# Kernel optimization log

Measured on AMD Instinct MI355X. Metric: run time of the kernel, lower is better.

## Reference

```python
import jax, jax.numpy as jnp
from jax import lax
import numpy as np

B = 2048; IMG = 28; K = 3; CIN = 1; HC = 32; LC = 16; WID = 64; HID = 64
LIS = IMG - 3 * (K - 1)           # 22: latent image size
FLAT = LIS * LIS * HC             # 15488
BLK = WID * LC                    # 1024: hypernet block size
T1 = 10.0; T0 = 0.0; NSTEP = 20   # fixed-step RK4 replaces adaptive dopri5
VAR = 0.1                         # p_z0 diagonal covariance


def _conv(x, w, b):  # w: [Cout,Cin,k,k], VALID conv, stride 1
    y = lax.conv_general_dilated(x, w, (1, 1), 'VALID',
                                 dimension_numbers=('NCHW', 'OIHW', 'NCHW'))
    return y + b[None, :, None, None]


def _convT(x, w, b):  # w: [Cin,Cout,k,k] (pytorch ConvTranspose2d layout)
    wf = jnp.flip(w, (2, 3)).transpose(1, 0, 2, 3)  # -> OIHW, spatially flipped
    y = lax.conv_general_dilated(x, wf, (1, 1), [(K - 1, K - 1), (K - 1, K - 1)],
                                 dimension_numbers=('NCHW', 'OIHW', 'NCHW'))
    return y + b[None, :, None, None]


def _forward(x, c0w, c0b, c1w, c1b, c2w, c2b, elw, elb, dlw, dlb,
             t0w, t0b, t1w, t1b, t2w, t2b, h1w, h1b, h2w, h2b, h3w, h3b):
    # ---- encoder (dropout in eval = identity) ----
    h = jnp.tanh(_conv(x, c0w, c0b))
    h = jnp.tanh(_conv(h, c1w, c1b))
    h = jnp.tanh(_conv(h, c2w, c2b))
    z1 = h.reshape(h.shape[0], -1) @ elw + elb          # [B, LC]
    # ---- decoder ----
    d = jnp.tanh(z1 @ dlw + dlb)                         # [B, FLAT]
    d = d.reshape(-1, HC, LIS, LIS)
    d = jnp.tanh(_convT(d, t0w, t0b))
    d = jnp.tanh(_convT(d, t1w, t1b))
    recon = _convT(d, t2w, t2b)                          # [B, CIN, 28, 28]

    # ---- CNF vector field with analytic trace ----
    def hyper(t):
        p = jnp.tanh(jnp.reshape(jnp.asarray(t, jnp.float32), (1, 1)) @ h1w + h1b)
        p = jnp.tanh(p @ h2w + h2b)
        p = (p @ h3w + h3b).reshape(-1)
        W = p[:BLK].reshape(WID, LC)
        U = p[BLK:2 * BLK].reshape(WID, LC) * jax.nn.sigmoid(p[2 * BLK:3 * BLK].reshape(WID, LC))
        Bb = p[3 * BLK:]                                 # [WID]
        return W, Bb, U

    def f(t, z):
        W, Bb, U = hyper(t)
        hh = jnp.tanh(jnp.einsum('bd,wd->wb', z, W) + Bb[:, None])   # [WID, B]
        dz = jnp.einsum('wb,wd->bd', hh, U) / WID                     # [B, LC]
        s = jnp.sum(W * U, axis=1)                                    # [WID]: sum_i W_w[i]U_w[i]
        tr = jnp.mean((1.0 - hh * hh) * s[:, None], axis=0)           # [B] analytic trace
        return dz, -tr[:, None]

    dt = (T0 - T1) / NSTEP

    def step(state, i):
        z, lp = state
        t = T1 + i * dt
        k1z, k1l = f(t, z)
        k2z, k2l = f(t + 0.5 * dt, z + 0.5 * dt * k1z)
        k3z, k3l = f(t + 0.5 * dt, z + 0.5 * dt * k2z)
        k4z, k4l = f(t + dt, z + dt * k3z)
        z = z + dt / 6.0 * (k1z + 2 * k2z + 2 * k3z + k4z)
        lp = lp + dt / 6.0 * (k1l + 2 * k2l + 2 * k3l + k4l)
        return (z, lp), None

    lp1 = jnp.zeros((z1.shape[0], 1), z1.dtype)
    (z0, lp0), _ = lax.scan(step, (z1, lp1), jnp.arange(NSTEP, dtype=jnp.float32))

    # MultivariateNormal(0, 0.1*I) log_prob
    logp = -0.5 * (LC * jnp.log(2 * jnp.pi) + LC * jnp.log(VAR) + jnp.sum(z0 * z0, -1) / VAR)
    x_probs = jnp.mean(logp - lp0[:, 0])
    return recon, x_probs


def setup_inputs() -> dict:
    key = jax.random.key(0)
    ks = jax.random.split(key, 16)
    n = jax.random.normal
    s = jnp.float32(0.05)
    z = jnp.zeros
    OUT3 = 3 * BLK + WID
    return {
        'x': n(ks[0], (B, CIN, IMG, IMG), jnp.float32),
        'c0w': n(ks[1], (HC, CIN, K, K)) * s, 'c0b': z((HC,)),
        'c1w': n(ks[2], (HC, HC, K, K)) * s, 'c1b': z((HC,)),
        'c2w': n(ks[3], (HC, HC, K, K)) * s, 'c2b': z((HC,)),
        'elw': n(ks[4], (FLAT, LC)) * s, 'elb': z((LC,)),
        'dlw': n(ks[5], (LC, FLAT)) * s, 'dlb': z((FLAT,)),
        't0w': n(ks[6], (HC, HC, K, K)) * s, 't0b': z((HC,)),
        't1w': n(ks[7], (HC, HC, K, K)) * s, 't1b': z((HC,)),
        't2w': n(ks[8], (HC, CIN, K, K)) * s, 't2b': z((CIN,)),
        'h1w': n(ks[9], (1, HID)) * s, 'h1b': z((HID,)),
        'h2w': n(ks[10], (HID, HID)) * s, 'h2b': z((HID,)),
        'h3w': n(ks[11], (HID, OUT3)) * s, 'h3b': z((OUT3,)),
    }


def reference(x, c0w, c0b, c1w, c1b, c2w, c2b, elw, elb, dlw, dlb,
              t0w, t0b, t1w, t1b, t2w, t2b, h1w, h1b, h2w, h2b, h3w, h3b):
    return _forward(x, c0w, c0b, c1w, c1b, c2w, c2b, elw, elb, dlw, dlb,
                    t0w, t0b, t1w, t1b, t2w, t2b, h1w, h1b, h2w, h2b, h3w, h3b)
```

## Files before the change

### kernel.cpp

```cpp
#include <hip/hip_runtime.h>
#include <math.h>

#define Bsz 2048

using bf16x8 = __attribute__((ext_vector_type(8))) short;
using f32x4  = __attribute__((ext_vector_type(4))) float;

__device__ __forceinline__ float fast_tanh(float x){
    float e = __expf(2.0f * x);
    return 1.0f - 2.0f / (e + 1.0f);
}
__device__ __forceinline__ float fast_sigmoid(float x){
    return 1.0f / (1.0f + __expf(-x));
}
__device__ __forceinline__ unsigned short f2b(float f){
    union { float f; unsigned u; } v; v.f = f;
    unsigned r = v.u + 0x7FFFu + ((v.u >> 16) & 1u);
    return (unsigned short)(r >> 16);
}
__device__ __forceinline__ float b2f(unsigned short s){
    union { unsigned u; float f; } v; v.u = ((unsigned)s) << 16;
    return v.f;
}

__device__ __forceinline__ float stage_t(int sidx){
    int i  = sidx >> 2, st = sidx & 3;
    float t = 10.0f - 0.5f * (float)i;
    if (st == 1 || st == 2) t -= 0.25f;
    else if (st == 3)       t -= 0.5f;
    return t;
}

__global__ void k_prep(const float* __restrict__ c1w, const float* __restrict__ c2w,
                       const float* __restrict__ t0w, const float* __restrict__ t1w,
                       const float* __restrict__ elw, const float* __restrict__ dlw,
                       const float* __restrict__ elb, const float* __restrict__ dlb,
                       const float* __restrict__ t2w,
                       unsigned short* __restrict__ wc1, unsigned short* __restrict__ wc2,
                       unsigned short* __restrict__ wt0, unsigned short* __restrict__ wt1,
                       unsigned short* __restrict__ t2wPk,
                       unsigned short* __restrict__ elwT, unsigned short* __restrict__ dlwT,
                       float* __restrict__ dlbT, float* __restrict__ z1, int full){
    int gsz = gridDim.x * 256;
    for (int i = blockIdx.x*256 + threadIdx.x; i < 9216; i += gsz){
        int ci = i & 31, co = (i >> 5) & 31, s = i >> 10;
        wc1[i] = f2b(c1w[(co*32 + ci)*9 + s]);
        wc2[i] = f2b(c2w[(co*32 + ci)*9 + s]);
        wt0[i] = f2b(t0w[(ci*32 + co)*9 + (8 - s)]);
        wt1[i] = f2b(t1w[(ci*32 + co)*9 + (8 - s)]);
    }
    if (!full) return;
    for (int i = blockIdx.x*256 + threadIdx.x; i < 288; i += gsz){
        int tap = i >> 5, ci = i & 31;
        int r = tap / 3, s = tap - r*3;
        t2wPk[i] = f2b(t2w[ci*9 + (2-r)*3 + (2-s)]);
    }
    for (int i = blockIdx.x*256 + threadIdx.x; i < 32768; i += gsz)
        z1[i] = elb[i & 15];
    for (int i = blockIdx.x*256 + threadIdx.x; i < 15488; i += gsz){
        int pos = i >> 5, ci = i & 31;
        dlbT[i] = dlb[ci*484 + pos];
    }
    for (int i = blockIdx.x*256 + threadIdx.x; i < 247808; i += gsz){
        int l = i / 15488, f2 = i - l*15488;
        int pos = f2 >> 5, ci = f2 & 31;
        elwT[i] = f2b(elw[(ci*484 + pos)*16 + l]);
    }
    for (int i = blockIdx.x*256 + threadIdx.x; i < 247808; i += gsz){
        int f2 = i >> 4, l = i & 15;
        int pos = f2 >> 5, ci = f2 & 31;
        dlwT[i] = f2b(dlw[l*15488 + ci*484 + pos]);
    }
}

__global__ void __launch_bounds__(256)
k_enc01(const float* __restrict__ x, const float* __restrict__ c0w,
        const float* __restrict__ c0b, const unsigned short* __restrict__ wc1,
        const float* __restrict__ c1b, unsigned short* __restrict__ A1,
        int cb){
    __shared__ __align__(16) unsigned short A0L[676*36];
    const int tid = threadIdx.x, b = blockIdx.x;
    const float* xin = x + (size_t)(cb + b)*784;

    for (int pos = tid; pos < 676; pos += 256){
        int y = pos / 26, xx = pos - y*26;
        float v[9];
#pragma unroll
        for (int r = 0; r < 3; r++)
#pragma unroll
            for (int s = 0; s < 3; s++)
                v[r*3+s] = xin[(y+r)*28 + xx + s];
        float acc[32];
#pragma unroll
        for (int co = 0; co < 32; co++) acc[co] = c0b[co];
#pragma unroll
        for (int k = 0; k < 9; k++)
#pragma unroll
            for (int co = 0; co < 32; co++)
                acc[co] += v[k] * c0w[co*9 + k];
        unsigned short* ob = A0L + pos*36;
#pragma unroll
        for (int g = 0; g < 8; g++){
            ushort4 o;
            o.x = f2b(fast_tanh(acc[g*4+0])); o.y = f2b(fast_tanh(acc[g*4+1]));
            o.z = f2b(fast_tanh(acc[g*4+2])); o.w = f2b(fast_tanh(acc[g*4+3]));
            *(ushort4*)(ob + g*4) = o;
        }
    }
    __syncthreads();

    const int wave = tid >> 6, lane = tid & 63;
    const int q = lane >> 4, nn = lane & 15;
    bf16x8 af[2][9];
#pragma unroll
    for (int mt = 0; mt < 2; mt++)
#pragma unroll
        for (int s = 0; s < 9; s++)
            af[mt][s] = *(const bf16x8*)(wc1 + s*1024 + (mt*16 + nn)*32 + q*8);
    float4 bc0 = *(const float4*)(c1b + q*4);
    float4 bc1 = *(const float4*)(c1b + 16 + q*4);
    unsigned short* outb = A1 + (size_t)b*25088;

    for (int t = wave; t < 36; t += 4){
        int pos = t*16 + nn;
        int oy = pos / 24, ox = pos - oy*24;
        const unsigned short* ib = A0L + (oy*26 + ox)*36 + q*8;
        f32x4 acc0 = {0.f,0.f,0.f,0.f}, acc1 = {0.f,0.f,0.f,0.f};
#pragma unroll
        for (int r = 0; r < 3; r++){
            bf16x8 b0 = *(const bf16x8*)(ib + (r*26 + 0)*36);
            bf16x8 b1 = *(const bf16x8*)(ib + (r*26 + 1)*36);
            bf16x8 b2 = *(const bf16x8*)(ib + (r*26 + 2)*36);
            acc0 = __builtin_amdgcn_mfma_f32_16x16x32_bf16(af[0][r*3+0], b0, acc0, 0,0,0);
            acc1 = __builtin_amdgcn_mfma_f32_16x16x32_bf16(af[1][r*3+0], b0, acc1, 0,0,0);
            acc0 = __builtin_amdgcn_mfma_f32_16x16x32_bf16(af[0][r*3+1], b1, acc0, 0,0,0);
            acc1 = __builtin_amdgcn_mfma_f32_16x16x32_bf16(af[1][r*3+1], b1, acc1, 0,0,0);
            acc0 = __builtin_amdgcn_mfma_f32_16x16x32_bf16(af[0][r*3+2], b2, acc0, 0,0,0);
            acc1 = __builtin_amdgcn_mfma_f32_16x16x32_bf16(af[1][r*3+2], b2, acc1, 0,0,0);
        }
        int opix = oy*24 + ox;
        ushort4 o0, o1;
        o0.x = f2b(fast_tanh(acc0[0] + bc0.x)); o0.y = f2b(fast_tanh(acc0[1] + bc0.y));
        o0.z = f2b(fast_tanh(acc0[2] + bc0.z)); o0.w = f2b(fast_tanh(acc0[3] + bc0.w));
        o1.x = f2b(fast_tanh(acc1[0] + bc1.x)); o1.y = f2b(fast_tanh(acc1[1] + bc1.y));
        o1.z = f2b(fast_tanh(acc1[2] + bc1.z)); o1.w = f2b(fast_tanh(acc1[3] + bc1.w));
        *(ushort4*)(outb + opix*32 + q*4)      = o0;
        *(ushort4*)(outb + opix*32 + 16 + q*4) = o1;
    }
}

template<int IL, int OL, int OW, int OOFF, int INS, int OUTS>
__global__ void __launch_bounds__(256)
k_convM(const unsigned short* __restrict__ in, const unsigned short* __restrict__ wg,
        const float* __restrict__ bias, unsigned short* __restrict__ out, int CH){
    constexpr int N  = OL * OL;
    constexpr int NT = (N + 15) / 16;
    const int tid = threadIdx.x;
    const int wave = tid >> 6, lane = tid & 63;
    const int q = lane >> 4, nn = lane & 15;
    const int nw = gridDim.x * 4;

    bf16x8 af[2][9];
#pragma unroll
    for (int mt = 0; mt < 2; mt++)
#pragma unroll
        for (int s = 0; s < 9; s++)
            af[mt][s] = *(const bf16x8*)(wg + s*1024 + (mt*16 + nn)*32 + q*8);
    float4 bc0 = *(const float4*)(bias + q*4);
    float4 bc1 = *(const float4*)(bias + 16 + q*4);

    for (int t = blockIdx.x*4 + wave; t < CH*NT; t += nw){
        int img = t / NT, tt = t - img*NT;
        const unsigned short* inb = in + (size_t)img * INS;
        unsigned short* outb = out + (size_t)img * OUTS;
        int pos = tt*16 + nn;
        int pc  = pos < N ? pos : N - 1;
        int oy = pc / OL, ox = pc - oy*OL;
        const unsigned short* ib = inb + (oy*IL + ox)*32 + q*8;
        f32x4 acc0 = {0.f,0.f,0.f,0.f}, acc1 = {0.f,0.f,0.f,0.f};
#pragma unroll
        for (int r = 0; r < 3; r++){
            bf16x8 b0 = *(const bf16x8*)(ib + (r*IL + 0)*32);
            bf16x8 b1 = *(const bf16x8*)(ib + (r*IL + 1)*32);
            bf16x8 b2 = *(const bf16x8*)(ib + (r*IL + 2)*32);
            acc0 = __builtin_amdgcn_mfma_f32_16x16x32_bf16(af[0][r*3+0], b0, acc0, 0,0,0);
            acc1 = __builtin_amdgcn_mfma_f32_16x16x32_bf16(af[1][r*3+0], b0, acc1, 0,0,0);
            acc0 = __builtin_amdgcn_mfma_f32_16x16x32_bf16(af[0][r*3+1], b1, acc0, 0,0,0);
            acc1 = __builtin_amdgcn_mfma_f32_16x16x32_bf16(af[1][r*3+1], b1, acc1, 0,0,0);
            acc0 = __builtin_amdgcn_mfma_f32_16x16x32_bf16(af[0][r*3+2], b2, acc0, 0,0,0);
            acc1 = __builtin_amdgcn_mfma_f32_16x16x32_bf16(af[1][r*3+2], b2, acc1, 0,0,0);
        }
        if (pos < N){
            int opix = oy*OW + ox + OOFF;
            ushort4 o0, o1;
            o0.x = f2b(fast_tanh(acc0[0] + bc0.x)); o0.y = f2b(fast_tanh(acc0[1] + bc0.y));
            o0.z = f2b(fast_tanh(acc0[2] + bc0.z)); o0.w = f2b(fast_tanh(acc0[3] + bc0.w));
            o1.x = f2b(fast_tanh(acc1[0] + bc1.x)); o1.y = f2b(fast_tanh(acc1[1] + bc1.y));
            o1.z = f2b(fast_tanh(acc1[2] + bc1.z)); o1.w = f2b(fast_tanh(acc1[3] + bc1.w));
            *(ushort4*)(outb + opix*32 + q*4)      = o0;
            *(ushort4*)(outb + opix*32 + 16 + q*4) = o1;
        }
    }
}

__global__ void __launch_bounds__(256)
k_encg(const unsigned short* __restrict__ A2, const unsigned short* __restrict__ elwT,
       float* __restrict__ z1, int cb, int CH){
    int wave = threadIdx.x >> 6, lane = threadIdx.x & 63;
    int q = lane >> 4, nn = lane & 15;
    int imgb = blockIdx.x*16;
    const unsigned short* ap = A2 + (size_t)(imgb + nn)*15488 + q*8;
    const unsigned short* bp = elwT + (size_t)nn*15488 + q*8;
    f32x4 acc = {0.f,0.f,0.f,0.f};
    int s0 = blockIdx.y*121;
#pragma unroll 2
    for (int s = s0 + wave; s < s0 + 121; s += 4){
        bf16x8 a = *(const bf16x8*)(ap + s*32);
        bf16x8 b = *(const bf16x8*)(bp + s*32);
        acc = __builtin_amdgcn_mfma_f32_16x16x32_bf16(a, b, acc, 0,0,0);
    }
    float* zp = z1 + (size_t)(cb + imgb)*16;
#pragma unroll
    for (int i = 0; i < 4; i++)
        atomicAdd(zp + (q*4 + i)*16 + nn, acc[i]);
}

__global__ void __launch_bounds__(256)
k_decgM(const float* __restrict__ z1, const unsigned short* __restrict__ dlwT,
        const float* __restrict__ dlbT, unsigned short* __restrict__ D0c, int cb){
    __shared__ float zb[16*17];
    const int tid = threadIdx.x;
    const int wave = tid >> 6, lane = tid & 63;
    const int q = lane >> 4, n = lane & 15;
    const int imgb = blockIdx.y*16;
    zb[(tid >> 4)*17 + (tid & 15)] = z1[(size_t)(cb + imgb + (tid >> 4))*16 + (tid & 15)];
    __syncthreads();

    bf16x8 zf;
    if (q < 2){
        unsigned short tmp[8];
#pragma unroll
        for (int j = 0; j < 8; j++) tmp[j] = f2b(zb[n*17 + q*8 + j]);
        zf = *(bf16x8*)tmp;
    } else {
        bf16x8 zz = {0,0,0,0,0,0,0,0}; zf = zz;
    }

#pragma unroll
    for (int ii = 0; ii < 4; ii++){
        int mt = blockIdx.x*16 + wave*4 + ii;
        if (mt >= 968) break;
        int mb = mt*16;
        bf16x8 afr;
        if (q < 2) afr = *(const bf16x8*)(dlwT + (size_t)(mb + n)*16 + q*8);
        else { bf16x8 zz = {0,0,0,0,0,0,0,0}; afr = zz; }
        f32x4 acc = {0.f,0.f,0.f,0.f};
        acc = __builtin_amdgcn_mfma_f32_16x16x32_bf16(afr, zf, acc, 0,0,0);
        float4 bias = *(const float4*)(dlbT + mb + q*4);
        ushort4 o;
        o.x = f2b(fast_tanh(acc[0] + bias.x));
        o.y = f2b(fast_tanh(acc[1] + bias.y));
        o.z = f2b(fast_tanh(acc[2] + bias.z));
        o.w = f2b(fast_tanh(acc[3] + bias.w));
        *(ushort4*)(D0c + (size_t)(imgb + n)*15488 + mb + q*4) = o;
    }
}

struct PM {
    bf16x8 Wf[4];
    bf16x8 Uf[2];
    float4 Bbf[4];
    float4 sf[4];
    float stot;
};
__device__ __forceinline__ void loadPM(const float* __restrict__ g, int lane, int q, PM& p){
    const unsigned short* gW = (const unsigned short*)g;
    const unsigned short* gU = (const unsigned short*)(g + 1024);
#pragma unroll
    for (int c = 0; c < 4; c++)
        p.Wf[c] = *(const bf16x8*)(gW + (c*64 + lane)*8);
#pragma unroll
    for (int kb = 0; kb < 2; kb++)
        p.Uf[kb] = *(const bf16x8*)(gU + (kb*64 + lane)*8);
#pragma unroll
    for (int c = 0; c < 4; c++){
        p.Bbf[c] = *(const float4*)(g + 1536 + c*16 + q*4);
        p.sf[c]  = *(const float4*)(g + 1600 + c*16 + q*4);
    }
    p.stot = g[1664];
}

__device__ __forceinline__ void cnf_body(const float* __restrict__ z1,
                                         const float* __restrict__ hyp,
                                         float* __restrict__ part, int bid,
                                         unsigned short* zsb, unsigned short* hhT){
    const int lane = threadIdx.x;
    const int q = lane >> 4, d = lane & 15;
    const float dt = -0.5f;

    float z[4], zacc[4], lacc[4], lp[4];
#pragma unroll
    for (int i = 0; i < 4; i++){
        z[i] = z1[(size_t)(bid*16 + q*4 + i)*16 + d];
        zacc[i] = 0.f; lacc[i] = 0.f; lp[i] = 0.f;
        zsb[(q*4 + i)*24 + d] = f2b(z[i]);
    }
    PM pm0, pm1;
    loadPM(hyp, lane, q, pm0);

#pragma unroll 2
    for (int sidx = 0; sidx < 80; sidx++){
        PM& cur = (sidx & 1) ? pm1 : pm0;
        PM& nxt = (sidx & 1) ? pm0 : pm1;
        if (sidx < 79) loadPM(hyp + (size_t)(sidx + 1)*2048, lane, q, nxt);

        bf16x8 zb;
        if (q < 2) zb = *(const bf16x8*)(zsb + d*24 + q*8);
        else { bf16x8 zz2 = {0,0,0,0,0,0,0,0}; zb = zz2; }

        f32x4 h0 = {0,0,0,0}, h1 = {0,0,0,0}, h2 = {0,0,0,0}, h3 = {0,0,0,0};
        h0 = __builtin_amdgcn_mfma_f32_16x16x32_bf16(cur.Wf[0], zb, h0, 0,0,0);
        h1 = __builtin_amdgcn_mfma_f32_16x16x32_bf16(cur.Wf[1], zb, h1, 0,0,0);
        h2 = __builtin_amdgcn_mfma_f32_16x16x32_bf16(cur.Wf[2], zb, h2, 0,0,0);
        h3 = __builtin_amdgcn_mfma_f32_16x16x32_bf16(cur.Wf[3], zb, h3, 0,0,0);

        float partial = 0.f;
        f32x4 hc[4] = {h0, h1, h2, h3};
#pragma unroll
        for (int c = 0; c < 4; c++){
            ushort4 o;
            float t0 = fast_tanh(hc[c][0] + cur.Bbf[c].x);
            float t1 = fast_tanh(hc[c][1] + cur.Bbf[c].y);
            float t2 = fast_tanh(hc[c][2] + cur.Bbf[c].z);
            float t3 = fast_tanh(hc[c][3] + cur.Bbf[c].w);
            partial += t0*t0*cur.sf[c].x + t1*t1*cur.sf[c].y
                     + t2*t2*cur.sf[c].z + t3*t3*cur.sf[c].w;
            o.x = f2b(t0); o.y = f2b(t1); o.z = f2b(t2); o.w = f2b(t3);
            *(ushort4*)(hhT + d*72 + c*16 + q*4) = o;
        }
        partial += __shfl_xor(partial, 16);
        partial += __shfl_xor(partial, 32);
        float trFull = (cur.stot - partial) * (1.f/64.f);

        bf16x8 a20 = *(const bf16x8*)(hhT + d*72 + q*8);
        bf16x8 a21 = *(const bf16x8*)(hhT + d*72 + 32 + q*8);
        f32x4 dzac = {0,0,0,0};
        dzac = __builtin_amdgcn_mfma_f32_16x16x32_bf16(a20, cur.Uf[0], dzac, 0,0,0);
        dzac = __builtin_amdgcn_mfma_f32_16x16x32_bf16(a21, cur.Uf[1], dzac, 0,0,0);

        int st = sidx & 3;
        float wgt = (st == 0 || st == 3) ? 1.f : 2.f;
#pragma unroll
        for (int i = 0; i < 4; i++){
            float dz = dzac[i] * (1.f/64.f);
            float dl = -__shfl(trFull, q*4 + i);
            zacc[i] += wgt * dz;
            lacc[i] += wgt * dl;
            float zsv;
            if (st < 3){
                float aa = (st == 2) ? 1.0f : 0.5f;
                zsv = z[i] + aa * dt * dz;
            } else {
                z[i]  += (dt/6.f) * zacc[i];
                lp[i] += (dt/6.f) * lacc[i];
                zsv = z[i];
                zacc[i] = 0.f; lacc[i] = 0.f;
            }
            zsb[(q*4 + i)*24 + d] = f2b(zsv);
        }
    }
    float sq[4];
#pragma unroll
    for (int i = 0; i < 4; i++) sq[i] = z[i]*z[i];
#pragma unroll
    for (int off = 1; off < 16; off <<= 1){
#pragma unroll
        for (int i = 0; i < 4; i++) sq[i] += __shfl_xor(sq[i], off, 16);
    }
    if (d == 0){
#pragma unroll
        for (int i = 0; i < 4; i++){
            float logp = -0.5f * (16.f*1.8378770664093453f
                                 + 16.f*(-2.302585092994046f) + sq[i]*10.f);
            part[bid*16 + q*4 + i] = logp - lp[i];
        }
    }
}

__global__ void __launch_bounds__(256)
k_dect0c(const unsigned short* __restrict__ D0c, const unsigned short* __restrict__ wt0,
         const float* __restrict__ t0b, unsigned short* __restrict__ D1,
         const float* __restrict__ z1, const float* __restrict__ hyp,
         float* __restrict__ part, int nCnf){
    __shared__ __align__(16) unsigned short D0L[676*36];
    __shared__ __align__(16) unsigned short zsbS[16*24];
    __shared__ __align__(16) unsigned short hhTS[16*72];
    const int tid = threadIdx.x;

    if (blockIdx.x < nCnf){
        if (tid >= 64) return;
        cnf_body(z1, hyp, part, blockIdx.x, zsbS, hhTS);
        return;
    }
    const int b = blockIdx.x - nCnf;
    unsigned short* d1b = D1 + (size_t)b*25088;
    {
        uint4 zq = {0,0,0,0};
        for (int p = tid; p < 676; p += 256){
            int y = p / 26, xx = p - y*26;
            if (y < 2 || y >= 24 || xx < 2 || xx >= 24){
                uint4* pt = (uint4*)(D0L + p*36);
                pt[0] = zq; pt[1] = zq; pt[2] = zq; pt[3] = zq;
            }
        }
        for (int p = tid; p < 784; p += 256){
            int y = p / 28, xx = p - y*28;
            if (y < 2 || y >= 26 || xx < 2 || xx >= 26){
                uint4* pt = (uint4*)(d1b + p*32);
                pt[0] = zq; pt[1] = zq; pt[2] = zq; pt[3] = zq;
            }
        }
    }
    {
        const uint4* src = (const uint4*)(D0c + (size_t)b*15488);
        for (int c = tid; c < 1936; c += 256){
            uint4 v = src[c];
            int pos = c >> 2, p8 = (c & 3)*8;
            int y = pos / 22, xx = pos - y*22;
            *(uint4*)(D0L + ((y+2)*26 + xx + 2)*36 + p8) = v;
        }
    }
    __syncthreads();

    const int wave = tid >> 6, lane = tid & 63;
    const int q = lane >> 4, nn = lane & 15;
    bf16x8 af[2][9];
#pragma unroll
    for (int mt = 0; mt < 2; mt++)
#pragma unroll
        for (int s = 0; s < 9; s++)
            af[mt][s] = *(const bf16x8*)(wt0 + s*1024 + (mt*16 + nn)*32 + q*8);
    float4 bc0 = *(const float4*)(t0b + q*4);
    float4 bc1 = *(const float4*)(t0b + 16 + q*4);

    for (int t = wave; t < 36; t += 4){
        int pos = t*16 + nn;
        int oy = pos / 24, ox = pos - oy*24;
        const unsigned short* ib = D0L + (oy*26 + ox)*36 + q*8;
        f32x4 acc0 = {0.f,0.f,0.f,0.f}, acc1 = {0.f,0.f,0.f,0.f};
#pragma unroll
        for (int r = 0; r < 3; r++){
            bf16x8 b0 = *(const bf16x8*)(ib + (r*26 + 0)*36);
            bf16x8 b1 = *(const bf16x8*)(ib + (r*26 + 1)*36);
            bf16x8 b2 = *(const bf16x8*)(ib + (r*26 + 2)*36);
            acc0 = __builtin_amdgcn_mfma_f32_16x16x32_bf16(af[0][r*3+0], b0, acc0, 0,0,0);
            acc1 = __builtin_amdgcn_mfma_f32_16x16x32_bf16(af[1][r*3+0], b0, acc1, 0,0,0);
            acc0 = __builtin_amdgcn_mfma_f32_16x16x32_bf16(af[0][r*3+1], b1, acc0, 0,0,0);
            acc1 = __builtin_amdgcn_mfma_f32_16x16x32_bf16(af[1][r*3+1], b1, acc1, 0,0,0);
            acc0 = __builtin_amdgcn_mfma_f32_16x16x32_bf16(af[0][r*3+2], b2, acc0, 0,0,0);
            acc1 = __builtin_amdgcn_mfma_f32_16x16x32_bf16(af[1][r*3+2], b2, acc1, 0,0,0);
        }
        int opix = oy*28 + ox + 58;
        ushort4 o0, o1;
        o0.x = f2b(fast_tanh(acc0[0] + bc0.x)); o0.y = f2b(fast_tanh(acc0[1] + bc0.y));
        o0.z = f2b(fast_tanh(acc0[2] + bc0.z)); o0.w = f2b(fast_tanh(acc0[3] + bc0.w));
        o1.x = f2b(fast_tanh(acc1[0] + bc1.x)); o1.y = f2b(fast_tanh(acc1[1] + bc1.y));
        o1.z = f2b(fast_tanh(acc1[2] + bc1.z)); o1.w = f2b(fast_tanh(acc1[3] + bc1.w));
        *(ushort4*)(d1b + opix*32 + q*4)      = o0;
        *(ushort4*)(d1b + opix*32 + 16 + q*4) = o1;
    }
}

__global__ void __launch_bounds__(256)
k_dect12(const unsigned short* __restrict__ D1, const unsigned short* __restrict__ wt1,
         const float* __restrict__ t1b, const unsigned short* __restrict__ t2wPk,
         const float* __restrict__ t2b, float* __restrict__ out,
         const float* __restrict__ part, int cb, int CH){
    __shared__ __align__(16) unsigned short D2L[900*40];
    const int tid = threadIdx.x, b = blockIdx.x;
    if (b >= CH){
        __shared__ float red[256];
        float s = 0.f;
#pragma unroll
        for (int k = 0; k < 8; k++) s += part[tid + k*256];
        red[tid] = s;
        __syncthreads();
        for (int st = 128; st > 0; st >>= 1){
            if (tid < st) red[tid] += red[tid + st];
            __syncthreads();
        }
        if (tid == 0) out[1605632] = red[0] * (1.f/2048.f);
        return;
    }
    const unsigned short* d1b = D1 + (size_t)b*25088;
    const int wave = tid >> 6, lane = tid & 63;
    const int q = lane >> 4, nn = lane & 15;

    {
        uint4 zq = {0,0,0,0};
        for (int p = tid; p < 900; p += 256){
            int y = p / 30, xx = p - y*30;
            if (y < 2 || y >= 28 || xx < 2 || xx >= 28){
                uint4* pt = (uint4*)(D2L + p*40);
                pt[0] = zq; pt[1] = zq; pt[2] = zq; pt[3] = zq;
            }
        }
    }
    {
        bf16x8 af[2][9];
#pragma unroll
        for (int mt = 0; mt < 2; mt++)
#pragma unroll
            for (int s = 0; s < 9; s++)
                af[mt][s] = *(const bf16x8*)(wt1 + s*1024 + (mt*16 + nn)*32 + q*8);
        float4 bc0 = *(const float4*)(t1b + q*4);
        float4 bc1 = *(const float4*)(t1b + 16 + q*4);

        for (int t = wave; t < 43; t += 4){
            int pos = t*16 + nn;
            int pc  = pos < 676 ? pos : 675;
            int oy = pc / 26, ox = pc - oy*26;
            const unsigned short* ib = d1b + (oy*28 + ox)*32 + q*8;
            f32x4 acc0 = {0.f,0.f,0.f,0.f}, acc1 = {0.f,0.f,0.f,0.f};
#pragma unroll
            for (int r = 0; r < 3; r++){
                bf16x8 b0 = *(const bf16x8*)(ib + (r*28 + 0)*32);
                bf16x8 b1 = *(const bf16x8*)(ib + (r*28 + 1)*32);
                bf16x8 b2 = *(const bf16x8*)(ib + (r*28 + 2)*32);
                acc0 = __builtin_amdgcn_mfma_f32_16x16x32_bf16(af[0][r*3+0], b0, acc0, 0,0,0);
                acc1 = __builtin_amdgcn_mfma_f32_16x16x32_bf16(af[1][r*3+0], b0, acc1, 0,0,0);
                acc0 = __builtin_amdgcn_mfma_f32_16x16x32_bf16(af[0][r*3+1], b1, acc0, 0,0,0);
                acc1 = __builtin_amdgcn_mfma_f32_16x16x32_bf16(af[1][r*3+1], b1, acc1, 0,0,0);
                acc0 = __builtin_amdgcn_mfma_f32_16x16x32_bf16(af[0][r*3+2], b2, acc0, 0,0,0);
                acc1 = __builtin_amdgcn_mfma_f32_16x16x32_bf16(af[1][r*3+2], b2, acc1, 0,0,0);
            }
            if (pos < 676){
                int opix = (oy + 2)*30 + ox + 2;
                ushort4 o0, o1;
                o0.x = f2b(fast_tanh(acc0[0] + bc0.x)); o0.y = f2b(fast_tanh(acc0[1] + bc0.y));
                o0.z = f2b(fast_tanh(acc0[2] + bc0.z)); o0.w = f2b(fast_tanh(acc0[3] + bc0.w));
                o1.x = f2b(fast_tanh(acc1[0] + bc1.x)); o1.y = f2b(fast_tanh(acc1[1] + bc1.y));
                o1.z = f2b(fast_tanh(acc1[2] + bc1.z)); o1.w = f2b(fast_tanh(acc1[3] + bc1.w));
                *(ushort4*)(D2L + opix*40 + q*4)      = o0;
                *(ushort4*)(D2L + opix*40 + 16 + q*4) = o1;
            }
        }
    }
    __syncthreads();

    {
        bf16x8 wf[9];
#pragma unroll
        for (int tap = 0; tap < 9; tap++)
            wf[tap] = *(const bf16x8*)(t2wPk + tap*32 + q*8);
        float t2b0 = t2b[0];
        for (int t = wave; t < 49; t += 4){
            int p = t*16 + nn;
            int y = p / 28, xx = p - y*28;
            const unsigned short* bbase = D2L + (y*30 + xx)*40 + q*8;
            f32x4 acc = {0.f,0.f,0.f,0.f};
#pragma unroll
            for (int r = 0; r < 3; r++){
                acc = __builtin_amdgcn_mfma_f32_16x16x32_bf16(wf[r*3+0],
                        *(const bf16x8*)(bbase + (r*30 + 0)*40), acc, 0,0,0);
                acc = __builtin_amdgcn_mfma_f32_16x16x32_bf16(wf[r*3+1],
                        *(const bf16x8*)(bbase + (r*30 + 1)*40), acc, 0,0,0);
                acc = __builtin_amdgcn_mfma_f32_16x16x32_bf16(wf[r*3+2],
                        *(const bf16x8*)(bbase + (r*30 + 2)*40), acc, 0,0,0);
            }
            if (q == 0)
                out[(size_t)(cb + b)*784 + p] = acc[0] + t2b0;
        }
    }
}

template<int LOUT, int INW, int OUTW, int OUTOFF>
__device__ __forceinline__ void conv_gemm(const unsigned short* __restrict__ Wg,
                                          const float* __restrict__ bias,
                                          const unsigned short* inL,
                                          unsigned short* outL, int tid){
    constexpr int N  = LOUT * LOUT;
    constexpr int NT = (N + 15) / 16;
    const int lane  = tid & 63;
    const int wave  = tid >> 6;
    const int mtile = wave & 1;
    const int quad  = lane >> 4;
    const int nn    = lane & 15;
    bf16x8 afr[9];
    const unsigned short* wp = Wg + (mtile*16 + nn)*32 + quad*8;
#pragma unroll
    for (int s = 0; s < 9; s++)
        afr[s] = *(const bf16x8*)(wp + s*1024);
    float4 bco = *(const float4*)(bias + mtile*16 + quad*4);
    for (int t = (wave >> 1); t < NT; t += 2){
        int pos = t*16 + nn;
        int pc  = pos < N ? pos : N - 1;
        int y = pc / LOUT, x = pc - y*LOUT;
        const unsigned short* ib = inL + (y*INW + x)*32 + quad*8;
        f32x4 acc = {0.f, 0.f, 0.f, 0.f};
#pragma unroll
        for (int r = 0; r < 3; r++)
#pragma unroll
            for (int s = 0; s < 3; s++)
                acc = __builtin_amdgcn_mfma_f32_16x16x32_bf16(
                        afr[r*3+s], *(const bf16x8*)(ib + (r*INW + s)*32), acc, 0, 0, 0);
        if (pos < N){
            ushort4 o;
            o.x = f2b(fast_tanh(acc[0] + bco.x));
            o.y = f2b(fast_tanh(acc[1] + bco.y));
            o.z = f2b(fast_tanh(acc[2] + bco.z));
            o.w = f2b(fast_tanh(acc[3] + bco.w));
            int opix = y*OUTW + x + OUTOFF;
            *(ushort4*)(outL + opix*32 + mtile*16 + quad*4) = o;
        }
    }
}

__global__ void __launch_bounds__(256)
k_enc_f(const float* __restrict__ x,
        const float* __restrict__ c0w, const float* __restrict__ c0b,
        const unsigned short* __restrict__ wc1, const float* __restrict__ c1b,
        const unsigned short* __restrict__ wc2, const float* __restrict__ c2b,
        const float* __restrict__ elw, const float* __restrict__ elb,
        float* __restrict__ z1){
    __shared__ float X[784];
    __shared__ __align__(16) unsigned short H0[21632];
    __shared__ __align__(16) unsigned short H1[18432];
    __shared__ __align__(16) unsigned short H2[15488];
    __shared__ float red[16*17];
    const int tid = threadIdx.x, b = blockIdx.x;
    for (int i = tid; i < 784; i += 256) X[i] = x[b*784 + i];
    __syncthreads();
    for (int pos = tid; pos < 676; pos += 256){
        int y = pos / 26, xx = pos - y*26;
        float v[9];
#pragma unroll
        for (int r = 0; r < 3; r++)
#pragma unroll
            for (int s = 0; s < 3; s++)
                v[r*3+s] = X[(y+r)*28 + xx + s];
#pragma unroll
        for (int g = 0; g < 8; g++){
            float a0 = c0b[g*4+0], a1 = c0b[g*4+1], a2 = c0b[g*4+2], a3 = c0b[g*4+3];
#pragma unroll
            for (int k = 0; k < 9; k++){
                a0 += v[k] * c0w[(g*4+0)*9 + k];
                a1 += v[k] * c0w[(g*4+1)*9 + k];
                a2 += v[k] * c0w[(g*4+2)*9 + k];
                a3 += v[k] * c0w[(g*4+3)*9 + k];
            }
            ushort4 o;
            o.x = f2b(fast_tanh(a0)); o.y = f2b(fast_tanh(a1));
            o.z = f2b(fast_tanh(a2)); o.w = f2b(fast_tanh(a3));
            *(ushort4*)(H0 + pos*32 + g*4) = o;
        }
    }
    __syncthreads();
    conv_gemm<24, 26, 24, 0>(wc1, c1b, H0, H1, tid);
    __syncthreads();
    conv_gemm<22, 24, 22, 0>(wc2, c2b, H1, H2, tid);
    __syncthreads();
    {
        int fg = tid >> 4, l = tid & 15;
        float a = 0.f;
        for (int ci = 0; ci < 32; ci++)
            for (int pos = fg; pos < 484; pos += 16)
                a += b2f(H2[pos*32 + ci]) * elw[(ci*484 + pos)*16 + l];
        red[fg*17 + l] = a;
        __syncthreads();
        if (tid < 16){
            float s = elb[tid];
#pragma unroll
            for (int g = 0; g < 16; g++) s += red[g*17 + tid];
            z1[b*16 + tid] = s;
        }
    }
}

__global__ void __launch_bounds__(256)
k_dec_f(const float* __restrict__ z1,
        const float* __restrict__ dlw, const float* __restrict__ dlb,
        const unsigned short* __restrict__ wt0, const float* __restrict__ t0b,
        const unsigned short* __restrict__ wt1, const float* __restrict__ t1b,
        const float* __restrict__ t2w, const float* __restrict__ t2b,
        float* __restrict__ out){
    __shared__ __align__(16) unsigned short D0[21632];
    __shared__ __align__(16) unsigned short D1[25088];
    __shared__ __align__(16) unsigned short D2[28800];
    const int tid = threadIdx.x, b = blockIdx.x;
    {
        uint4 zq = {0,0,0,0};
        for (int i = tid; i < 2704; i += 256) ((uint4*)D0)[i] = zq;
        for (int i = tid; i < 3136; i += 256) ((uint4*)D1)[i] = zq;
        for (int i = tid; i < 3600; i += 256) ((uint4*)D2)[i] = zq;
    }
    float zz[16];
#pragma unroll
    for (int l = 0; l < 16; l++) zz[l] = z1[b*16 + l];
    __syncthreads();
    for (int f = tid; f < 15488; f += 256){
        float a = dlb[f];
#pragma unroll
        for (int l = 0; l < 16; l++) a += zz[l] * dlw[l*15488 + f];
        int ci = f / 484, pos = f - ci*484;
        int y = pos / 22, xx = pos - y*22;
        D0[((y+2)*26 + xx + 2)*32 + ci] = f2b(fast_tanh(a));
    }
    __syncthreads();
    conv_gemm<24, 26, 28, 58>(wt0, t0b, D0, D1, tid);
    __syncthreads();
    conv_gemm<26, 28, 30, 62>(wt1, t1b, D1, D2, tid);
    __syncthreads();
    for (int o = tid; o < 784; o += 256){
        int y = o / 28, xx = o - y*28;
        float a = t2b[0];
#pragma unroll
        for (int r = 0; r < 3; r++)
#pragma unroll
            for (int s = 0; s < 3; s++){
                const unsigned short* pp = D2 + ((y+r)*30 + xx + s)*32;
                int wi = (2-r)*3 + (2-s);
#pragma unroll
                for (int g = 0; g < 4; g++){
                    bf16x8 h = *(const bf16x8*)(pp + g*8);
#pragma unroll
                    for (int j = 0; j < 8; j++)
                        a += b2f((unsigned short)h[j]) * t2w[(g*8+j)*9 + wi];
                }
            }
        out[(size_t)b*784 + o] = a;
    }
}

__global__ void __launch_bounds__(64)
k_hyp1(const float* __restrict__ h1w, const float* __restrict__ h1b,
       const float* __restrict__ h2w, const float* __restrict__ h2b,
       float* __restrict__ p2ws){
    __shared__ float p1l[64];
    int sidx = blockIdx.x, tid = threadIdx.x;
    float t = stage_t(sidx);
    p1l[tid] = fast_tanh(t * h1w[tid] + h1b[tid]);
    __syncthreads();
    float a0 = h2b[tid], a1 = 0.f, a2 = 0.f, a3 = 0.f;
#pragma unroll
    for (int k = 0; k < 64; k += 4){
        a0 += p1l[k]   * h2w[(k)*64   + tid];
        a1 += p1l[k+1] * h2w[(k+1)*64 + tid];
        a2 += p1l[k+2] * h2w[(k+2)*64 + tid];
        a3 += p1l[k+3] * h2w[(k+3)*64 + tid];
    }
    p2ws[sidx*64 + tid] = fast_tanh((a0 + a1) + (a2 + a3));
}

__global__ void __launch_bounds__(256)
k_hyp2(const float* __restrict__ p2ws, const float* __restrict__ h3w,
       const float* __restrict__ h3b, float* __restrict__ p3ws){
    __shared__ float p2l[64];
    int sidx = blockIdx.y, tid = threadIdx.x;
    if (tid < 64) p2l[tid] = p2ws[sidx*64 + tid];
    __syncthreads();
    int m = blockIdx.x*256 + tid;
    if (m >= 3136) return;
    const float* hp = h3w + m;
    float a0 = h3b[m], a1 = 0.f, a2 = 0.f, a3 = 0.f;
#pragma unroll
    for (int k = 0; k < 64; k += 4){
        a0 += p2l[k]   * hp[(size_t)(k)*3136];
        a1 += p2l[k+1] * hp[(size_t)(k+1)*3136];
        a2 += p2l[k+2] * hp[(size_t)(k+2)*3136];
        a3 += p2l[k+3] * hp[(size_t)(k+3)*3136];
    }
    p3ws[(size_t)sidx*3200 + m] = (a0 + a1) + (a2 + a3);
}

__global__ void __launch_bounds__(256)
k_hyp3(const float* __restrict__ p3ws, float* __restrict__ hyp){
    __shared__ float sred[64];
    int sidx = blockIdx.x, tid = threadIdx.x;
    const float* p3 = p3ws + (size_t)sidx*3200;
    float* g = hyp + (size_t)sidx*2048;
    unsigned short* gW = (unsigned short*)g;
    unsigned short* gU = (unsigned short*)(g + 1024);
    {
        int lane = tid & 63, c = tid >> 6;
        int q = lane >> 4, m = lane & 15;
        ushort4 o0 = {0,0,0,0}, o1 = {0,0,0,0};
        if (q < 2){
            const float* wp = p3 + (c*16 + m)*16 + q*8;
            o0.x = f2b(wp[0]); o0.y = f2b(wp[1]); o0.z = f2b(wp[2]); o0.w = f2b(wp[3]);
            o1.x = f2b(wp[4]); o1.y = f2b(wp[5]); o1.z = f2b(wp[6]); o1.w = f2b(wp[7]);
        }
        *(ushort4*)(gW + tid*8)     = o0;
        *(ushort4*)(gW + tid*8 + 4) = o1;
    }
    if (tid < 128){
        int lane = tid & 63, kb = tid >> 6;
        int q = lane >> 4, d = lane & 15;
        unsigned short uo[8];
#pragma unroll
        for (int j = 0; j < 8; j++){
            int w = kb*32 + q*8 + j;
            float u = p3[1024 + w*16 + d] * fast_sigmoid(p3[2048 + w*16 + d]);
            uo[j] = f2b(u);
        }
        *(ushort4*)(gU + tid*8)     = *(ushort4*)&uo[0];
        *(ushort4*)(gU + tid*8 + 4) = *(ushort4*)&uo[4];
    } else if (tid < 192){
        int w = tid - 128;
        g[1536 + w] = p3[3072 + w];
    } else {
        int w = tid - 192;
        float s = 0.f;
#pragma unroll
        for (int d = 0; d < 16; d++){
            float u = p3[1024 + w*16 + d] * fast_sigmoid(p3[2048 + w*16 + d]);
            s += p3[w*16 + d] * u;
        }
        g[1600 + w] = s;
        sred[w] = s;
    }
    __syncthreads();
    if (tid == 0){
        float st = 0.f;
#pragma unroll
        for (int w = 0; w < 64; w++) st += sred[w];
        g[1664] = st;
    }
}

__global__ void k_hyper(const float* __restrict__ h1w, const float* __restrict__ h1b,
                        const float* __restrict__ h2w, const float* __restrict__ h2b,
                        const float* __restrict__ h3w, const float* __restrict__ h3b,
                        float* __restrict__ hyp){
    int sidx = blockIdx.x;
    float t = stage_t(sidx);
    __shared__ float p1[64], p2[64];
    __shared__ float p3[3136];
    int tid = threadIdx.x;
    if (tid < 64) p1[tid] = fast_tanh(t * h1w[tid] + h1b[tid]);
    __syncthreads();
    if (tid < 64){
        float a = h2b[tid];
#pragma unroll
        for (int k = 0; k < 64; k++) a += p1[k] * h2w[k*64 + tid];
        p2[tid] = fast_tanh(a);
    }
    __syncthreads();
    for (int m = tid; m < 3136; m += 256){
        float a = h3b[m];
#pragma unroll
        for (int k = 0; k < 64; k++) a += p2[k] * h3w[k*3136 + m];
        p3[m] = a;
    }
    __syncthreads();
    float* g = hyp + (size_t)sidx * 2304;
    for (int m = tid; m < 1024; m += 256){
        g[m] = p3[m];
        float u = p3[1024 + m] * fast_sigmoid(p3[2048 + m]);
        g[1024 + (m & 15)*64 + (m >> 4)] = u;
        p3[1024 + m] = u;
    }
    if (tid < 64) g[2048 + tid] = p3[3072 + tid];
    __syncthreads();
    if (tid < 64){
        float s = 0.f;
#pragma unroll
        for (int d = 0; d < 16; d++) s += p3[tid*16 + d] * p3[1024 + tid*16 + d];
        g[2112 + tid] = s;
    }
}

struct PF { float4 Wr[4]; float4 Ur[4]; float Bb, sw; };
__device__ __forceinline__ void load_pf(const float* __restrict__ g,
                                        int lane, int q, int d, PF& p){
    const float4* w4 = (const float4*)(g + lane*16);
    p.Wr[0] = w4[0]; p.Wr[1] = w4[1]; p.Wr[2] = w4[2]; p.Wr[3] = w4[3];
    const float4* u4 = (const float4*)(g + 1024 + d*64 + q*16);
    p.Ur[0] = u4[0]; p.Ur[1] = u4[1]; p.Ur[2] = u4[2]; p.Ur[3] = u4[3];
    p.Bb = g[2048 + lane];
    p.sw = g[2112 + lane];
}
__global__ void __launch_bounds__(64)
k_cnf_f(const float* __restrict__ z1, const float* __restrict__ hyp,
        float* __restrict__ part){
    __shared__ __align__(16) float zsl[16];
    __shared__ __align__(16) float hhl[64];
    const int lane = threadIdx.x;
    const int q = lane >> 4, d = lane & 15;
    const float dt = -0.5f;
    float z  = z1[(size_t)blockIdx.x*16 + d];
    float zs = z;
    float lp = 0.f, zacc = 0.f, lacc = 0.f;
    if (lane < 16) zsl[lane] = zs;
    PF cur, nxt;
    load_pf(hyp, lane, q, d, cur);
    for (int sidx = 0; sidx < 80; sidx++){
        __syncthreads();
        if (sidx < 79) load_pf(hyp + (size_t)(sidx + 1)*2304, lane, q, d, nxt);
        const float4* zp = (const float4*)zsl;
        float4 z0 = zp[0], z1v = zp[1], z2 = zp[2], z3 = zp[3];
        float a = cur.Bb;
        a += z0.x*cur.Wr[0].x + z0.y*cur.Wr[0].y + z0.z*cur.Wr[0].z + z0.w*cur.Wr[0].w;
        a += z1v.x*cur.Wr[1].x + z1v.y*cur.Wr[1].y + z1v.z*cur.Wr[1].z + z1v.w*cur.Wr[1].w;
        a += z2.x*cur.Wr[2].x + z2.y*cur.Wr[2].y + z2.z*cur.Wr[2].z + z2.w*cur.Wr[2].w;
        a += z3.x*cur.Wr[3].x + z3.y*cur.Wr[3].y + z3.z*cur.Wr[3].z + z3.w*cur.Wr[3].w;
        float hh = fast_tanh(a);
        float e = (1.f - hh*hh) * cur.sw;
#pragma unroll
        for (int off = 1; off < 64; off <<= 1)
            e += __shfl_xor(e, off);
        hhl[lane] = hh;
        __syncthreads();
        const float4* hp = (const float4*)(hhl + q*16);
        float4 h0 = hp[0], h1 = hp[1], h2 = hp[2], h3 = hp[3];
        float dzp = 0.f;
        dzp += h0.x*cur.Ur[0].x + h0.y*cur.Ur[0].y + h0.z*cur.Ur[0].z + h0.w*cur.Ur[0].w;
        dzp += h1.x*cur.Ur[1].x + h1.y*cur.Ur[1].y + h1.z*cur.Ur[1].z + h1.w*cur.Ur[1].w;
        dzp += h2.x*cur.Ur[2].x + h2.y*cur.Ur[2].y + h2.z*cur.Ur[2].z + h2.w*cur.Ur[2].w;
        dzp += h3.x*cur.Ur[3].x + h3.y*cur.Ur[3].y + h3.z*cur.Ur[3].z + h3.w*cur.Ur[3].w;
        dzp += __shfl_xor(dzp, 16);
        dzp += __shfl_xor(dzp, 32);
        float dz = dzp * (1.f/64.f);
        float dl = -e  * (1.f/64.f);
        int st = sidx & 3;
        float wgt = (st == 0 || st == 3) ? 1.f : 2.f;
        zacc += wgt * dz;
        lacc += wgt * dl;
        if (st < 3){
            float aa = (st == 2) ? 1.0f : 0.5f;
            zs = z + aa * dt * dz;
        } else {
            z  += (dt/6.f) * zacc;
            lp += (dt/6.f) * lacc;
            zs = z;
            zacc = 0.f; lacc = 0.f;
        }
        if (lane < 16) zsl[lane] = zs;
        cur = nxt;
    }
    float sq = z * z;
#pragma unroll
    for (int off = 1; off < 16; off <<= 1) sq += __shfl_xor(sq, off, 16);
    float logp = -0.5f * (16.f*1.8378770664093453f + 16.f*(-2.302585092994046f) + sq*10.f);
    if (lane == 0) part[blockIdx.x] = logp - lp;
}

__global__ void k_final(const float* __restrict__ part, float* __restrict__ out){
    __shared__ float red[256];
    int tid = threadIdx.x;
    float s = 0.f;
#pragma unroll
    for (int k = 0; k < 8; k++) s += part[tid + k*256];
    red[tid] = s;
    __syncthreads();
    for (int st = 128; st > 0; st >>= 1){
        if (tid < st) red[tid] += red[tid + st];
        __syncthreads();
    }
    if (tid == 0) out[1605632] = red[0] * (1.f/2048.f);
}

extern "C" void kernel_launch(void* const* d_in, const int* in_sizes, int n_in,
                              void* d_out, int out_size, void* d_ws, size_t ws_size,
                              hipStream_t stream){
    const float* x   = (const float*)d_in[0];
    const float* c0w = (const float*)d_in[1];
    const float* c0b = (const float*)d_in[2];
    const float* c1w = (const float*)d_in[3];
    const float* c1b = (const float*)d_in[4];
    const float* c2w = (const float*)d_in[5];
    const float* c2b = (const float*)d_in[6];
    const float* elw = (const float*)d_in[7];
    const float* elb = (const float*)d_in[8];
    const float* dlw = (const float*)d_in[9];
    const float* dlb = (const float*)d_in[10];
    const float* t0w = (const float*)d_in[11];
    const float* t0b = (const float*)d_in[12];
    const float* t1w = (const float*)d_in[13];
    const float* t1b = (const float*)d_in[14];
    const float* t2w = (const float*)d_in[15];
    const float* t2b = (const float*)d_in[16];
    const float* h1w = (const float*)d_in[17];
    const float* h1b = (const float*)d_in[18];
    const float* h2w = (const float*)d_in[19];
    const float* h2b = (const float*)d_in[20];
    const float* h3w = (const float*)d_in[21];
    const float* h3b = (const float*)d_in[22];

    float* ws   = (float*)d_ws;
    float* z1   = ws;
    float* hyp  = z1 + 32768;
    float* part = hyp + 184320;
    float* p2ws = part + 2048;
    float* p3ws = p2ws + 5120;
    float* dlbT = p3ws + 256000;
    unsigned short* wc1  = (unsigned short*)(dlbT + 15488);
    unsigned short* wc2  = wc1 + 9216;
    unsigned short* wt0  = wc2 + 9216;
    unsigned short* wt1  = wt0 + 9216;
    unsigned short* t2wPk = wt1 + 9216;
    unsigned short* elwT = t2wPk + 288;
    unsigned short* dlwT = elwT + 247808;
    unsigned short* act  = dlwT + 247808;
    float* rec  = (float*)d_out;

    const size_t MISC = 3048512;
    int CH = 0;
    const int cands[6] = {2048, 1024, 512, 256, 128, 64};
    for (int c = 0; c < 6; c++){
        size_t need = MISC + (size_t)cands[c] * 81152;
        if (need <= ws_size){ CH = cands[c]; break; }
    }

    if (CH == 0){
        k_hyper<<<80, 256, 0, stream>>>(h1w, h1b, h2w, h2b, h3w, h3b, hyp);
        k_prep <<<64,   256, 0, stream>>>(c1w, c2w, t0w, t1w, elw, dlw, elb, dlb, t2w,
                                          wc1, wc2, wt0, wt1, t2wPk, wt1, wt1, z1, z1, 0);
        k_enc_f<<<2048, 256, 0, stream>>>(x, c0w, c0b, wc1, c1b, wc2, c2b, elw, elb, z1);
        k_cnf_f<<<2048,  64, 0, stream>>>(z1, hyp, part);
        k_dec_f<<<2048, 256, 0, stream>>>(z1, dlw, dlb, wt0, t0b, wt1, t1b, t2w, t2b, rec);
        k_final<<<1,    256, 0, stream>>>(part, rec);
        return;
    }

    k_hyp1<<<80,           64, 0, stream>>>(h1w, h1b, h2w, h2b, p2ws);
    k_hyp2<<<dim3(13,80), 256, 0, stream>>>(p2ws, h3w, h3b, p3ws);
    k_hyp3<<<80,          256, 0, stream>>>(p3ws, hyp);

    k_prep<<<64, 256, 0, stream>>>(c1w, c2w, t0w, t1w, elw, dlw, elb, dlb, t2w,
                                   wc1, wc2, wt0, wt1, t2wPk, elwT, dlwT, dlbT, z1, 1);

    unsigned short* X = act;
    unsigned short* Y = X + (size_t)CH*25088;

    for (int cb = 0; cb < Bsz; cb += CH){
        int last = (cb + CH >= Bsz);
        int nCnf = last ? 128 : 0;
        k_enc01<<<CH, 256, 0, stream>>>(x, c0w, c0b, wc1, c1b, X, cb);
        k_convM<24,22,22,0, 25088, 15488><<<(CH*31 + 15)/16, 256, 0, stream>>>(X, wc2, c2b, Y, CH);
        k_encg<<<dim3(CH/16, 4), 256, 0, stream>>>(Y, elwT, z1, cb, CH);
        k_decgM<<<dim3(61, CH/16), 256, 0, stream>>>(z1, dlwT, dlbT, Y, cb);
        k_dect0c<<<CH + nCnf, 256, 0, stream>>>(Y, wt0, t0b, X, z1, hyp, part, nCnf);
        k_dect12<<<CH + (last ? 1 : 0), 256, 0, stream>>>(X, wt1, t1b, t2wPk, t2b, rec, part, cb, CH);
    }
}
```

Measured before the change: 551.4 us.

## Split CNF integration across two decoder kernels and stage input image in LDS

The 80-stage RK4 CNF integration, which previously ran entirely inside the t0 decoder kernel alongside the conv blocks, is split into two halves. The first 40 stages run in k_dect0c and the last 40 in k_dect12, with the intermediate z and log-prob state passed through new workspace buffers. This shortens the serial CNF tail that could dominate each kernel, and the final reduction moves to a separate k_final launch. The first encoder conv now also stages the 28x28 input image in shared memory instead of reading global memory repeatedly, at the cost of an extra barrier and an extra kernel launch.

Result: slower. 567.4 us (+2.9%).

```diff
diff --git a/kernel.cpp b/kernel.cpp
--- a/kernel.cpp
+++ b/kernel.cpp
@@ -79,8 +79,12 @@
         const float* __restrict__ c1b, unsigned short* __restrict__ A1,
         int cb){
     __shared__ __align__(16) unsigned short A0L[676*36];
+    __shared__ float X[784];
     const int tid = threadIdx.x, b = blockIdx.x;
     const float* xin = x + (size_t)(cb + b)*784;
+
+    for (int i = tid; i < 784; i += 256) X[i] = xin[i];
+    __syncthreads();
 
     for (int pos = tid; pos < 676; pos += 256){
         int y = pos / 26, xx = pos - y*26;
@@ -89,7 +93,7 @@
         for (int r = 0; r < 3; r++)
 #pragma unroll
             for (int s = 0; s < 3; s++)
-                v[r*3+s] = xin[(y+r)*28 + xx + s];
+                v[r*3+s] = X[(y+r)*28 + xx + s];
         float acc[32];
 #pragma unroll
         for (int co = 0; co < 32; co++) acc[co] = c0b[co];
@@ -290,9 +294,13 @@
     p.stot = g[1664];
 }
 
-__device__ __forceinline__ void cnf_body(const float* __restrict__ z1,
+__device__ __forceinline__ void cnf_half(const float* __restrict__ zin,
+                                         const float* __restrict__ lpin,
+                                         float* __restrict__ zout,
+                                         float* __restrict__ lpout,
+                                         float* __restrict__ part,
                                          const float* __restrict__ hyp,
-                                         float* __restrict__ part, int bid,
+                                         int bid, int s0, int s1, int finalize,
                                          unsigned short* zsb, unsigned short* hhT){
     const int lane = threadIdx.x;
     const int q = lane >> 4, d = lane & 15;
@@ -301,18 +309,19 @@
     float z[4], zacc[4], lacc[4], lp[4];
 #pragma unroll
     for (int i = 0; i < 4; i++){
-        z[i] = z1[(size_t)(bid*16 + q*4 + i)*16 + d];
-        zacc[i] = 0.f; lacc[i] = 0.f; lp[i] = 0.f;
+        z[i] = zin[(size_t)(bid*16 + q*4 + i)*16 + d];
+        lp[i] = lpin ? lpin[bid*16 + q*4 + i] : 0.f;
+        zacc[i] = 0.f; lacc[i] = 0.f;
         zsb[(q*4 + i)*24 + d] = f2b(z[i]);
     }
     PM pm0, pm1;
-    loadPM(hyp, lane, q, pm0);
+    loadPM(hyp + (size_t)s0*2048, lane, q, pm0);
 
 #pragma unroll 2
-    for (int sidx = 0; sidx < 80; sidx++){
+    for (int sidx = s0; sidx < s1; sidx++){
         PM& cur = (sidx & 1) ? pm1 : pm0;
         PM& nxt = (sidx & 1) ? pm0 : pm1;
-        if (sidx < 79) loadPM(hyp + (size_t)(sidx + 1)*2048, lane, q, nxt);
+        if (sidx + 1 < 80) loadPM(hyp + (size_t)(sidx + 1)*2048, lane, q, nxt);
 
         bf16x8 zb;
         if (q < 2) zb = *(const bf16x8*)(zsb + d*24 + q*8);
@@ -369,6 +378,14 @@
             zsb[(q*4 + i)*24 + d] = f2b(zsv);
         }
     }
+    if (!finalize){
+#pragma unroll
+        for (int i = 0; i < 4; i++){
+            zout[(size_t)(bid*16 + q*4 + i)*16 + d] = z[i];
+            if (d == 0) lpout[bid*16 + q*4 + i] = lp[i];
+        }
+        return;
+    }
     float sq[4];
 #pragma unroll
     for (int i = 0; i < 4; i++) sq[i] = z[i]*z[i];
@@ -391,7 +408,7 @@
 k_dect0c(const unsigned short* __restrict__ D0c, const unsigned short* __restrict__ wt0,
          const float* __restrict__ t0b, unsigned short* __restrict__ D1,
          const float* __restrict__ z1, const float* __restrict__ hyp,
-         float* __restrict__ part, int nCnf){
+         float* __restrict__ zmid, float* __restrict__ lpmid, int nCnf){
     __shared__ __align__(16) unsigned short D0L[676*36];
     __shared__ __align__(16) unsigned short zsbS[16*24];
     __shared__ __align__(16) unsigned short hhTS[16*72];
@@ -399,7 +416,8 @@
 
     if (blockIdx.x < nCnf){
         if (tid >= 64) return;
-        cnf_body(z1, hyp, part, blockIdx.x, zsbS, hhTS);
+        cnf_half(z1, nullptr, zmid, lpmid, nullptr, hyp,
+                 blockIdx.x, 0, 40, 0, zsbS, hhTS);
         return;
     }
     const int b = blockIdx.x - nCnf;
@@ -475,23 +493,20 @@
 k_dect12(const unsigned short* __restrict__ D1, const unsigned short* __restrict__ wt1,
          const float* __restrict__ t1b, const unsigned short* __restrict__ t2wPk,
          const float* __restrict__ t2b, float* __restrict__ out,
-         const float* __restrict__ part, int cb, int CH){
+         const float* __restrict__ zmid, const float* __restrict__ lpmid,
+         const float* __restrict__ hyp, float* __restrict__ part,
+         int cb, int nCnf){
     __shared__ __align__(16) unsigned short D2L[900*40];
-    const int tid = threadIdx.x, b = blockIdx.x;
-    if (b >= CH){
-        __shared__ float red[256];
-        float s = 0.f;
-#pragma unroll
-        for (int k = 0; k < 8; k++) s += part[tid + k*256];
-        red[tid] = s;
-        __syncthreads();
-        for (int st = 128; st > 0; st >>= 1){
-            if (tid < st) red[tid] += red[tid + st];
-            __syncthreads();
-        }
-        if (tid == 0) out[1605632] = red[0] * (1.f/2048.f);
+    __shared__ __align__(16) unsigned short zsbS[16*24];
+    __shared__ __align__(16) unsigned short hhTS[16*72];
+    const int tid = threadIdx.x;
+    if (blockIdx.x < nCnf){
+        if (tid >= 64) return;
+        cnf_half(zmid, lpmid, nullptr, nullptr, part, hyp,
+                 blockIdx.x, 40, 80, 1, zsbS, hhTS);
         return;
     }
+    const int b = blockIdx.x - nCnf;
     const unsigned short* d1b = D1 + (size_t)b*25088;
     const int wave = tid >> 6, lane = tid & 63;
     const int q = lane >> 4, nn = lane & 15;
@@ -991,7 +1006,9 @@
     float* z1   = ws;
     float* hyp  = z1 + 32768;
     float* part = hyp + 184320;
-    float* p2ws = part + 2048;
+    float* zmid = part + 2048;
+    float* lpmid= zmid + 32768;
+    float* p2ws = lpmid + 2048;
     float* p3ws = p2ws + 5120;
     float* dlbT = p3ws + 256000;
     unsigned short* wc1  = (unsigned short*)(dlbT + 15488);
@@ -1004,7 +1021,7 @@
     unsigned short* act  = dlwT + 247808;
     float* rec  = (float*)d_out;
 
-    const size_t MISC = 3048512;
+    const size_t MISC = 3187776;
     int CH = 0;
     const int cands[6] = {2048, 1024, 512, 256, 128, 64};
     for (int c = 0; c < 6; c++){
@@ -1040,7 +1057,9 @@
         k_convM<24,22,22,0, 25088, 15488><<<(CH*31 + 15)/16, 256, 0, stream>>>(X, wc2, c2b, Y, CH);
         k_encg<<<dim3(CH/16, 4), 256, 0, stream>>>(Y, elwT, z1, cb, CH);
         k_decgM<<<dim3(61, CH/16), 256, 0, stream>>>(z1, dlwT, dlbT, Y, cb);
-        k_dect0c<<<CH + nCnf, 256, 0, stream>>>(Y, wt0, t0b, X, z1, hyp, part, nCnf);
-        k_dect12<<<CH + (last ? 1 : 0), 256, 0, stream>>>(X, wt1, t1b, t2wPk, t2b, rec, part, cb, CH);
-    }
-}
+        k_dect0c<<<CH + nCnf, 256, 0, stream>>>(Y, wt0, t0b, X, z1, hyp, zmid, lpmid, nCnf);
+        k_dect12<<<CH + nCnf, 256, 0, stream>>>(X, wt1, t1b, t2wPk, t2b, rec,
+                                                zmid, lpmid, hyp, part, cb, nCnf);
+    }
+    k_final<<<1, 256, 0, stream>>>(part, rec);
+}
```
